# Kernel tuning notes

Hardware: AMD Instinct MI355X
Metric: run time of the kernel (lower is better)

The kernel has to match this reference:

```python
import math
import jax, jax.numpy as jnp
import numpy as np

D_MODEL = 1024
N_HEADS = 16
HEAD_DIM = D_MODEL // N_HEADS  # 64
KV_DIM = int(HEAD_DIM * 0.25)  # 16
B, T = 2, 2048


def setup_inputs() -> dict:
    key = jax.random.key(0)
    ks = jax.random.split(key, 12)
    s_in = 1.0 / math.sqrt(D_MODEL)
    s_kv = 1.0 / math.sqrt(KV_DIM)
    x = jax.random.normal(ks[0], (B, T, D_MODEL), dtype=jnp.float32)
    # causal mask: 1 where attention allowed
    mask = jnp.tril(jnp.ones((T, T), dtype=jnp.int32))[None, None, :, :]
    return {
        "x": x,
        "Wc": jax.random.uniform(ks[1], (D_MODEL, KV_DIM), jnp.float32, -s_in, s_in),
        "bc": jax.random.uniform(ks[2], (KV_DIM,), jnp.float32, -s_in, s_in),
        "Wk": jax.random.uniform(ks[3], (KV_DIM, D_MODEL), jnp.float32, -s_kv, s_kv),
        "bk": jax.random.uniform(ks[4], (D_MODEL,), jnp.float32, -s_kv, s_kv),
        "Wv": jax.random.uniform(ks[5], (KV_DIM, D_MODEL), jnp.float32, -s_kv, s_kv),
        "bv": jax.random.uniform(ks[6], (D_MODEL,), jnp.float32, -s_kv, s_kv),
        "Wq": jax.random.uniform(ks[7], (D_MODEL, D_MODEL), jnp.float32, -s_in, s_in),
        "bq": jax.random.uniform(ks[8], (D_MODEL,), jnp.float32, -s_in, s_in),
        "Wo": jax.random.uniform(ks[9], (D_MODEL, D_MODEL), jnp.float32, -s_in, s_in),
        "bo": jax.random.uniform(ks[10], (D_MODEL,), jnp.float32, -s_in, s_in),
        "mask": mask,
    }


def reference(x, Wc, bc, Wk, bk, Wv, bv, Wq, bq, Wo, bo, mask):
    Bsz, Tlen, C = x.shape
    kv_compressed = x @ Wc + bc                      # [B, T, kv_dim]
    k = kv_compressed @ Wk + bk                      # [B, T, C]
    v = kv_compressed @ Wv + bv                      # [B, T, C]
    q = x @ Wq + bq                                  # [B, T, C]
    # split heads -> [B, H, T, hd]
    def split(t):
        return t.reshape(Bsz, Tlen, N_HEADS, HEAD_DIM).transpose(0, 2, 1, 3)
    q, k, v = split(q), split(k), split(v)
    scale = 1.0 / math.sqrt(HEAD_DIM)
    attn = jnp.einsum("bhqd,bhkd->bhqk", q, k) * scale  # [B, H, T, T]
    attn = jnp.where(mask == 0, jnp.float32(-jnp.inf), attn)
    attn = jax.nn.softmax(attn, axis=-1)
    y = jnp.einsum("bhqk,bhkd->bhqd", attn, v)       # [B, H, T, hd]
    y = y.transpose(0, 2, 1, 3).reshape(Bsz, Tlen, C)
    return y @ Wo + bo
```

## Files before the change

### kernel.cpp

```cpp
#include <hip/hip_runtime.h>
#include <hip/hip_bf16.h>
#include <math.h>

#define TT 2048
#define BB 2
#define DM 1024
#define NH 16
#define HD 64
#define KVD 16
#define BT (BB*TT)
#define QP 256

typedef short short8  __attribute__((ext_vector_type(8)));
typedef short short4v __attribute__((ext_vector_type(4)));
typedef float f32x4   __attribute__((ext_vector_type(4)));
typedef float f32x16  __attribute__((ext_vector_type(16)));

static __device__ __forceinline__ short f2bf(float f) {
    union { float f; unsigned u; } v; v.f = f;
    unsigned r = v.u + 0x7fffu + ((v.u >> 16) & 1u);
    return (short)(r >> 16);
}

static __device__ __forceinline__ float fexp2(float x) {
#if __has_builtin(__builtin_amdgcn_exp2f)
    return __builtin_amdgcn_exp2f(x);
#else
    return exp2f(x);
#endif
}

__global__ __launch_bounds__(256) void prep_all(
    const float* __restrict__ Wq, const float* __restrict__ Wk,
    const float* __restrict__ bq,
    const float* __restrict__ Wv, const float* __restrict__ Wo,
    const float* __restrict__ bv,
    const float* __restrict__ x,  const float* __restrict__ Wc,
    const float* __restrict__ bc,
    short* __restrict__ Wqt, float* __restrict__ bqp,
    short* __restrict__ Wvot, float* __restrict__ bop_part,
    short* __restrict__ x_bf, short* __restrict__ kvc16, short* __restrict__ kvcT)
{
    __shared__ __align__(16) char smem[20736];
    int bid = blockIdx.x, tid = threadIdx.x;
    if (bid < 256) {
        const float SC = 0.18033688011112042f;
        float (*wk)[64] = (float(*)[64])smem;
        float (*wq)[65] = (float(*)[65])(smem + 4096);
        int h = bid >> 4, dt = bid & 15;
        int d0 = dt * 64;
        for (int idx = tid; idx < 1024; idx += 256) {
            int j = idx >> 6, e = idx & 63;
            wk[j][e] = Wk[j*DM + h*HD + e];
        }
        #pragma unroll
        for (int i = 0; i < 16; ++i) {
            int idx = i*256 + tid;
            int r = idx >> 6, e = idx & 63;
            wq[r][e] = Wq[(d0 + r)*DM + h*HD + e];
        }
        __syncthreads();
        int r = tid & 63, j0 = (tid >> 6) * 4;
        float a0=0.f, a1=0.f, a2=0.f, a3=0.f;
        #pragma unroll 8
        for (int e = 0; e < 64; ++e) {
            float a = wq[r][e];
            a0 += a * wk[j0+0][e];
            a1 += a * wk[j0+1][e];
            a2 += a * wk[j0+2][e];
            a3 += a * wk[j0+3][e];
        }
        Wqt[(h*16 + j0+0)*DM + d0 + r] = f2bf(a0 * SC);
        Wqt[(h*16 + j0+1)*DM + d0 + r] = f2bf(a1 * SC);
        Wqt[(h*16 + j0+2)*DM + d0 + r] = f2bf(a2 * SC);
        Wqt[(h*16 + j0+3)*DM + d0 + r] = f2bf(a3 * SC);
        if (dt == 0 && tid < 16) {
            int j = tid;
            float acc = 0.f;
            #pragma unroll 8
            for (int e = 0; e < 64; ++e) acc += bq[h*HD + e] * wk[j][e];
            bqp[h*16 + j] = acc * SC;
        }
    } else if (bid < 320) {
        float (*wv)[64] = (float(*)[64])smem;
        float* bvs = (float*)(smem + 4096);
        int hb = bid - 256;
        int h = hb >> 2, nt = hb & 3;
        int n = nt*256 + tid;
        for (int idx = tid; idx < 1024; idx += 256) {
            int j = idx >> 6, e = idx & 63;
            wv[j][e] = Wv[j*DM + h*HD + e];
        }
        if (tid < 64) bvs[tid] = bv[h*HD + tid];
        __syncthreads();
        float acc[16];
        #pragma unroll
        for (int j = 0; j < 16; ++j) acc[j] = 0.f;
        float bacc = 0.f;
        #pragma unroll 4
        for (int e = 0; e < 64; ++e) {
            float wo = Wo[(h*HD + e)*DM + n];
            bacc += bvs[e] * wo;
            #pragma unroll
            for (int j = 0; j < 16; ++j) acc[j] += wv[j][e] * wo;
        }
        short8 o0, o1;
        #pragma unroll
        for (int j = 0; j < 8; ++j) { o0[j] = f2bf(acc[j]); o1[j] = f2bf(acc[j+8]); }
        *(short8*)(Wvot + n*QP + h*16)     = o0;
        *(short8*)(Wvot + n*QP + h*16 + 8) = o1;
        bop_part[h*DM + n] = bacc;
    } else {
        float (*xs)[DM]      = (float(*)[DM])smem;
        float (*part)[16][17] = (float(*)[16][17])(smem + 16384);
        int t0 = (bid - 320) * 4;
        #pragma unroll
        for (int i = 0; i < 4; ++i) {
            float4 xv = *(const float4*)(x + (t0+i)*DM + tid*4);
            *(float4*)(&xs[i][tid*4]) = xv;
            short4v xb;
            xb[0]=f2bf(xv.x); xb[1]=f2bf(xv.y); xb[2]=f2bf(xv.z); xb[3]=f2bf(xv.w);
            *(short4v*)(x_bf + (t0+i)*DM + tid*4) = xb;
        }
        __syncthreads();
        int g = tid >> 4, n = tid & 15;
        float a0=0.f, a1=0.f, a2=0.f, a3=0.f;
        #pragma unroll 4
        for (int k = 0; k < 64; ++k) {
            float wc = Wc[(g*64 + k)*KVD + n];
            a0 += xs[0][g*64+k]*wc; a1 += xs[1][g*64+k]*wc;
            a2 += xs[2][g*64+k]*wc; a3 += xs[3][g*64+k]*wc;
        }
        part[0][g][n]=a0; part[1][g][n]=a1; part[2][g][n]=a2; part[3][g][n]=a3;
        __syncthreads();
        if (tid < 64) {
            int i = tid >> 4, nn = tid & 15;
            float s = bc[nn];
            #pragma unroll
            for (int gg = 0; gg < 16; ++gg) s += part[i][gg][nn];
            short v = f2bf(s);
            int t = t0 + i;
            kvc16[t*16 + nn] = v;
            int b = t >> 11, tl = t & (TT-1);
            kvcT[(b*32 + nn)*TT + tl]      = v;
            kvcT[(b*32 + 16 + nn)*TT + tl] = (nn == 0) ? (short)0x3F80 : (short)0;
        }
    }
}

__global__ __launch_bounds__(256) void attn(
    const short* __restrict__ x_bf, const short* __restrict__ Wqt,
    const float* __restrict__ bqp,
    const short* __restrict__ kvc16, const short* __restrict__ kvcT,
    short* __restrict__ u_bf)
{
    int bid = blockIdx.x;
    int pp = bid >> 5, bh = bid & 31;
    int b = bh >> 4, h = bh & 15;
    int tid = threadIdx.x;
    int w = tid >> 6, lane = tid & 63;
    int l15 = lane & 15, g = lane >> 4;
    int l31 = lane & 31, hi = lane >> 5;

    __shared__ __align__(16) char smem[10752];
    short (*qtile)[16]    = (short(*)[16])smem;
    float (*ulds)[32][17] = (float(*)[32][17])(smem + 2048);

    {
        int itile = w >> 1, half = w & 1;
        int qb = (itile ? (63 - pp) : pp) * 32 + half * 16;
        f32x4 qa = {0.f,0.f,0.f,0.f};
        const short* ar = x_bf + (b*TT + qb + l15)*DM + 8*g;
        const short* br = Wqt  + (h*16 + l15)*DM + 8*g;
        #pragma unroll 4
        for (int k0 = 0; k0 < DM; k0 += 32) {
            short8 a  = *(const short8*)(ar + k0);
            short8 bb = *(const short8*)(br + k0);
            qa = __builtin_amdgcn_mfma_f32_16x16x32_bf16(a, bb, qa, 0, 0, 0);
        }
        float bias = bqp[h*16 + l15];
        #pragma unroll
        for (int r = 0; r < 4; ++r)
            qtile[w*16 + 4*g + r][l15] = f2bf(qa[r] + bias);
    }
    __syncthreads();

    const short* kbase = kvc16 + (b*TT + l31)*16 + 8*hi;
    const short* vrow  = kvcT + (b*32 + l31)*TT + 8*hi;

    #pragma unroll 1
    for (int it = 0; it < 2; ++it) {
        int qt = it ? (63 - pp) : pp;
        int qbase = qt * 32;
        short8 qf = *(const short8*)(&qtile[it*32 + l31][8*hi]);

        int ntiles = qt + 1;
        int t0 = (w * ntiles) >> 2;
        int t1 = ((w + 1) * ntiles) >> 2;

        f32x16 u;
        f32x16 zf;
        #pragma unroll
        for (int r = 0; r < 16; ++r) { u[r] = 0.f; zf[r] = 0.f; }

        if (t0 < t1) {
            int kv0 = t0 << 5;
            short8 kf  = *(const short8*)(kbase + kv0*16);
            short8 va  = *(const short8*)(vrow + kv0);
            short8 vb  = *(const short8*)(vrow + kv0 + 16);
            for (int kt = t0; kt < t1; ++kt) {
                short8 kf_n = kf, va_n = va, vb_n = vb;
                if (kt + 1 < t1) {
                    int kvn = (kt + 1) << 5;
                    kf_n = *(const short8*)(kbase + kvn*16);
                    va_n = *(const short8*)(vrow + kvn);
                    vb_n = *(const short8*)(vrow + kvn + 16);
                }
                f32x16 st = __builtin_amdgcn_mfma_f32_32x32x16_bf16(kf, qf, zf, 0, 0, 0);
                if (kt == qt) {
                    #pragma unroll
                    for (int r = 0; r < 16; ++r) {
                        int kvl = (r & 3) + 8*(r >> 2) + 4*hi;
                        if (kvl > l31) st[r] = -INFINITY;
                    }
                }
                float p[16];
                #pragma unroll
                for (int r = 0; r < 16; ++r) p[r] = fexp2(st[r]);
                int wd[8];
                #pragma unroll
                for (int i = 0; i < 8; ++i) {
                    asm("v_cvt_pk_bf16_f32 %0, %1, %2" : "=v"(wd[i]) : "v"(p[2*i]), "v"(p[2*i+1]));
                }
                int c00 = wd[0], c02 = wd[2], c01 = wd[1], c03 = wd[3];
                int c10 = wd[4], c12 = wd[6], c11 = wd[5], c13 = wd[7];
                asm volatile("v_permlane32_swap_b32 %0, %1" : "+v"(c00), "+v"(c02));
                asm volatile("v_permlane32_swap_b32 %0, %1" : "+v"(c01), "+v"(c03));
                asm volatile("v_permlane32_swap_b32 %0, %1" : "+v"(c10), "+v"(c12));
                asm volatile("v_permlane32_swap_b32 %0, %1" : "+v"(c11), "+v"(c13));
                union { int i4[4]; short8 s8; } pa0, pa1;
                pa0.i4[0]=c00; pa0.i4[1]=c01; pa0.i4[2]=c02; pa0.i4[3]=c03;
                pa1.i4[0]=c10; pa1.i4[1]=c11; pa1.i4[2]=c12; pa1.i4[3]=c13;
                u = __builtin_amdgcn_mfma_f32_32x32x16_bf16(pa0.s8, va, u, 0, 0, 0);
                u = __builtin_amdgcn_mfma_f32_32x32x16_bf16(pa1.s8, vb, u, 0, 0, 0);
                kf = kf_n; va = va_n; vb = vb_n;
            }
        }

        #pragma unroll
        for (int r = 0; r < 16; ++r) {
            int q = (r & 3) + 8*(r >> 2) + 4*hi;
            if (l31 < 17) ulds[w][q][l31] = u[r];
        }
        __syncthreads();
        #pragma unroll
        for (int e = 0; e < 2; ++e) {
            int idx = tid*2 + e;
            int q = idx >> 4, lat = idx & 15;
            float us = ulds[0][q][lat] + ulds[1][q][lat] + ulds[2][q][lat] + ulds[3][q][lat];
            float dd = ulds[0][q][16]  + ulds[1][q][16]  + ulds[2][q][16]  + ulds[3][q][16];
            u_bf[(b*TT + qbase + q)*QP + h*16 + lat] = f2bf(us / dd);
        }
        __syncthreads();
    }
}

__global__ __launch_bounds__(256) void ogemm(
    const short* __restrict__ u_bf, const short* __restrict__ Wvot,
    const float* __restrict__ bo, const float* __restrict__ bop_part,
    float* __restrict__ out)
{
    int bid = blockIdx.x;
    int w = threadIdx.x >> 6, lane = threadIdx.x & 63;
    int l15 = lane & 15, g = lane >> 4;
    int m0 = (bid >> 4)*64 + w*16;
    int nb = (bid & 15)*64;
    __shared__ float bs[64];
    int tid = threadIdx.x;
    if (tid < 64) {
        int n = nb + tid;
        float s = bo[n];
        #pragma unroll
        for (int hh = 0; hh < 16; ++hh) s += bop_part[hh*DM + n];
        bs[tid] = s;
    }
    __syncthreads();
    f32x4 acc[4];
    #pragma unroll
    for (int nt = 0; nt < 4; ++nt) acc[nt] = (f32x4){0.f,0.f,0.f,0.f};
    const short* arow = u_bf + (m0 + l15)*QP + 8*g;
    for (int k0 = 0; k0 < QP; k0 += 32) {
        short8 a = *(const short8*)(arow + k0);
        #pragma unroll
        for (int nt = 0; nt < 4; ++nt) {
            short8 bfr = *(const short8*)(Wvot + (nb + nt*16 + l15)*QP + k0 + 8*g);
            acc[nt] = __builtin_amdgcn_mfma_f32_16x16x32_bf16(a, bfr, acc[nt], 0, 0, 0);
        }
    }
    #pragma unroll
    for (int nt = 0; nt < 4; ++nt) {
        int n = nb + nt*16 + l15;
        float bias = bs[nt*16 + l15];
        #pragma unroll
        for (int r = 0; r < 4; ++r)
            out[(m0 + 4*g + r)*DM + n] = acc[nt][r] + bias;
    }
}

extern "C" void kernel_launch(void* const* d_in, const int* in_sizes, int n_in,
                              void* d_out, int out_size, void* d_ws, size_t ws_size,
                              hipStream_t stream) {
    const float* x  = (const float*)d_in[0];
    const float* Wc = (const float*)d_in[1];
    const float* bc = (const float*)d_in[2];
    const float* Wk = (const float*)d_in[3];
    const float* Wv = (const float*)d_in[5];
    const float* bv = (const float*)d_in[6];
    const float* Wq = (const float*)d_in[7];
    const float* bq = (const float*)d_in[8];
    const float* Wo = (const float*)d_in[9];
    const float* bo = (const float*)d_in[10];
    float* out = (float*)d_out;

    char* ws = (char*)d_ws;
    short* x_bf     = (short*)(ws);
    short* Wqt      = (short*)(ws + (8u<<20));
    short* Wvot     = (short*)(ws + (8u<<20) + (512u<<10));
    float* bqp      = (float*)(ws + (9u<<20));
    float* bop_part = (float*)(ws + (9u<<20) + 8192);
    short* kvc16    = (short*)(ws + (9u<<20) + (512u<<10));
    short* kvcT     = (short*)(ws + (9u<<20) + (768u<<10));
    short* u_bf     = (short*)(ws + (14u<<20));

    hipLaunchKernelGGL(prep_all, dim3(1344), dim3(256), 0, stream,
                       Wq, Wk, bq, Wv, Wo, bv, x, Wc, bc,
                       Wqt, bqp, Wvot, bop_part, x_bf, kvc16, kvcT);
    hipLaunchKernelGGL(attn,     dim3(1024), dim3(256), 0, stream,
                       x_bf, Wqt, bqp, kvc16, kvcT, u_bf);
    hipLaunchKernelGGL(ogemm,    dim3(1024), dim3(256), 0, stream,
                       u_bf, Wvot, bo, bop_part, out);
}
```

Before: 89.62 us.

## Tile V layout per key block and software-pipeline the QK MFMA

Changes the transposed compressed-KV buffer to a tiled layout, so each 32-key tile's V fragment is a contiguous 1 KB chunk instead of strided rows across the whole sequence. In the attention loop, the next tile's score MFMA is issued before the current tile's PV MFMAs, so matrix work can overlap the exp and pack step and the load latency. This costs extra live registers for the carried score accumulator and V operands, which may lower occupancy.

```diff
diff --git a/kernel.cpp b/kernel.cpp
--- a/kernel.cpp
+++ b/kernel.cpp
@@ -142,8 +142,11 @@
             int t = t0 + i;
             kvc16[t*16 + nn] = v;
             int b = t >> 11, tl = t & (TT-1);
-            kvcT[(b*32 + nn)*TT + tl]      = v;
-            kvcT[(b*32 + 16 + nn)*TT + tl] = (nn == 0) ? (short)0x3F80 : (short)0;
+            int kt = tl >> 5, kvl = tl & 31;
+            int half = kvl >> 4, k16 = kvl & 15;
+            int base = ((b*64 + kt)*2 + half) * 512;
+            kvcT[base + nn*16 + k16]        = v;
+            kvcT[base + (16+nn)*16 + k16]   = (nn == 0) ? (short)0x3F80 : (short)0;
         }
     }
 }
@@ -186,7 +189,7 @@
     __syncthreads();
 
     const short* kbase = kvc16 + (b*TT + l31)*16 + 8*hi;
-    const short* vrow  = kvcT + (b*32 + l31)*TT + 8*hi;
+    const short* vbase = kvcT + b*65536 + l31*16 + 8*hi;
 
     #pragma unroll 1
     for (int it = 0; it < 2; ++it) {
@@ -204,29 +207,31 @@
         for (int r = 0; r < 16; ++r) { u[r] = 0.f; zf[r] = 0.f; }
 
         if (t0 < t1) {
-            int kv0 = t0 << 5;
-            short8 kf  = *(const short8*)(kbase + kv0*16);
-            short8 va  = *(const short8*)(vrow + kv0);
-            short8 vb  = *(const short8*)(vrow + kv0 + 16);
+            short8 kf = *(const short8*)(kbase + (t0 << 9));
+            const short* vt0 = vbase + (t0 << 10);
+            short8 va = *(const short8*)(vt0);
+            short8 vb = *(const short8*)(vt0 + 512);
+            f32x16 st = __builtin_amdgcn_mfma_f32_32x32x16_bf16(kf, qf, zf, 0, 0, 0);
+
             for (int kt = t0; kt < t1; ++kt) {
-                short8 kf_n = kf, va_n = va, vb_n = vb;
+                short8 va_c = va, vb_c = vb;
+                f32x16 st_c = st;
                 if (kt + 1 < t1) {
-                    int kvn = (kt + 1) << 5;
-                    kf_n = *(const short8*)(kbase + kvn*16);
-                    va_n = *(const short8*)(vrow + kvn);
-                    vb_n = *(const short8*)(vrow + kvn + 16);
+                    const short* vn = vbase + ((kt + 1) << 10);
+                    kf = *(const short8*)(kbase + ((kt + 1) << 9));
+                    va = *(const short8*)(vn);
+                    vb = *(const short8*)(vn + 512);
                 }
-                f32x16 st = __builtin_amdgcn_mfma_f32_32x32x16_bf16(kf, qf, zf, 0, 0, 0);
                 if (kt == qt) {
                     #pragma unroll
                     for (int r = 0; r < 16; ++r) {
                         int kvl = (r & 3) + 8*(r >> 2) + 4*hi;
-                        if (kvl > l31) st[r] = -INFINITY;
+                        if (kvl > l31) st_c[r] = -INFINITY;
                     }
                 }
                 float p[16];
                 #pragma unroll
-                for (int r = 0; r < 16; ++r) p[r] = fexp2(st[r]);
+                for (int r = 0; r < 16; ++r) p[r] = fexp2(st_c[r]);
                 int wd[8];
                 #pragma unroll
                 for (int i = 0; i < 8; ++i) {
@@ -241,9 +246,10 @@
                 union { int i4[4]; short8 s8; } pa0, pa1;
                 pa0.i4[0]=c00; pa0.i4[1]=c01; pa0.i4[2]=c02; pa0.i4[3]=c03;
                 pa1.i4[0]=c10; pa1.i4[1]=c11; pa1.i4[2]=c12; pa1.i4[3]=c13;
-                u = __builtin_amdgcn_mfma_f32_32x32x16_bf16(pa0.s8, va, u, 0, 0, 0);
-                u = __builtin_amdgcn_mfma_f32_32x32x16_bf16(pa1.s8, vb, u, 0, 0, 0);
-                kf = kf_n; va = va_n; vb = vb_n;
+                if (kt + 1 < t1)
+                    st = __builtin_amdgcn_mfma_f32_32x32x16_bf16(kf, qf, zf, 0, 0, 0);
+                u = __builtin_amdgcn_mfma_f32_32x32x16_bf16(pa0.s8, va_c, u, 0, 0, 0);
+                u = __builtin_amdgcn_mfma_f32_32x32x16_bf16(pa1.s8, vb_c, u, 0, 0, 0);
             }
         }
 
```

New measurement: 84.51 us. 5.7% less time.
